# Kernel tuning notes

Hardware: AMD Instinct MI355X
Metric: run time of the kernel (lower is better)

The kernel has to match this reference:

```python
import jax, jax.numpy as jnp
import numpy as np

N_NODES = 100000
N_EDGES = 1600000
IN_FEATS = 128
H1 = 256
H2 = 256
N_CLASSES = 64


def setup_inputs() -> dict:
    key = jax.random.key(0)
    ks = jax.random.split(key, 12)
    x = jax.random.normal(ks[0], (N_NODES, IN_FEATS), dtype=jnp.float32)
    src = jax.random.randint(ks[1], (N_EDGES,), 0, N_NODES, dtype=jnp.int64 if jax.config.jax_enable_x64 else jnp.int32)
    dst = jax.random.randint(ks[2], (N_EDGES,), 0, N_NODES, dtype=jnp.int64 if jax.config.jax_enable_x64 else jnp.int32)
    def lin(kw, kb, fan_in, fan_out):
        bound = 1.0 / np.sqrt(fan_in)
        W = jax.random.uniform(kw, (fan_out, fan_in), minval=-bound, maxval=bound, dtype=jnp.float32)
        b = jax.random.uniform(kb, (fan_out,), minval=-bound, maxval=bound, dtype=jnp.float32)
        return W, b
    W1, b1 = lin(ks[3], ks[4], 2 * IN_FEATS, H1)
    W2, b2 = lin(ks[5], ks[6], 2 * H1, H2)
    W3, b3 = lin(ks[7], ks[8], 2 * H2, N_CLASSES)
    return {"x": x, "src": src, "dst": dst,
            "W1": W1, "b1": b1, "W2": W2, "b2": b2, "W3": W3, "b3": b3}


def _sage_conv(h, src, dst, W, b):
    # message = copy from src node, reduce = mean at dst node (DGL copy_u + mean)
    m = jnp.take(h, src, axis=0)                                  # [E, d]
    s = jax.ops.segment_sum(m, dst, num_segments=N_NODES)         # [N, d]
    deg = jax.ops.segment_sum(jnp.ones((m.shape[0],), h.dtype), dst,
                              num_segments=N_NODES)               # [N]
    h_N = s / jnp.maximum(deg, 1.0)[:, None]                      # isolated nodes -> 0 (DGL behavior)
    h_total = jnp.concatenate([h, h_N], axis=1)                   # [N, 2d]
    return h_total @ W.T + b                                      # dropout inactive at eval (p=0.05)


def reference(x, src, dst, W1, b1, W2, b2, W3, b3):
    h = jax.nn.relu(_sage_conv(x, src, dst, W1, b1))
    h = jax.nn.relu(_sage_conv(h, src, dst, W2, b2))
    return _sage_conv(h, src, dst, W3, b3)
```

## Files before the change

kernel.cpp:

```cpp
#include <hip/hip_runtime.h>
#include <hip/hip_bf16.h>
#include <cstdint>
#include <cstddef>

#define N_NODES 100000
#define N_EDGES 1600000
#define NBUCK   64
#define NPB     1563
#define NB_E    ((N_EDGES + 4095) / 4096)

typedef __attribute__((ext_vector_type(8))) short short8;
typedef __attribute__((ext_vector_type(4))) float floatx4;

__device__ inline float bf_lo(unsigned int u) { return __uint_as_float(u << 16); }
__device__ inline float bf_hi(unsigned int u) { return __uint_as_float(u & 0xffff0000u); }
__device__ inline unsigned short f2bf(float f) {
  unsigned int u = __float_as_uint(f);
  u += 0x7fffu + ((u >> 16) & 1u);
  return (unsigned short)(u >> 16);
}

__global__ void cvt_f32_bf16(const float* __restrict__ in,
                             unsigned short* __restrict__ out, int n4) {
  int t = blockIdx.x * blockDim.x + threadIdx.x;
  if (t >= n4) return;
  float4 v = ((const float4*)in)[t];
  ushort4 o;
  o.x = f2bf(v.x); o.y = f2bf(v.y); o.z = f2bf(v.z); o.w = f2bf(v.w);
  ((ushort4*)out)[t] = o;
}

__global__ void cvt_w3cat(const float* __restrict__ W3, unsigned short* __restrict__ out) {
  int t = blockIdx.x * blockDim.x + threadIdx.x;
  if (t >= 128 * 256 / 4) return;
  int idx4 = t * 4;
  int r = idx4 >> 8, c = idx4 & 255;
  float4 v = *(const float4*)(W3 + (size_t)(r & 63) * 512 + (r >> 6) * 256 + c);
  ushort4 o;
  o.x = f2bf(v.x); o.y = f2bf(v.y); o.z = f2bf(v.z); o.w = f2bf(v.w);
  *(ushort4*)(out + (size_t)r * 256 + c) = o;
}

__device__ inline int wave_incl_scan(int v, int lane) {
#pragma unroll
  for (int off = 1; off < 64; off <<= 1) {
    int t = __shfl_up(v, off, 64);
    if (lane >= off) v += t;
  }
  return v;
}

__global__ __launch_bounds__(256)
void pass1a_kernel(const int* __restrict__ dst, int* __restrict__ bucketCount) {
  __shared__ int hist[NBUCK];
  if (threadIdx.x < NBUCK) hist[threadIdx.x] = 0;
  __syncthreads();
#pragma unroll
  for (int i = 0; i < 16; ++i) {
    int e = blockIdx.x * 4096 + i * 256 + threadIdx.x;
    if (e < N_EDGES) atomicAdd(&hist[dst[e] / NPB], 1);
  }
  __syncthreads();
  if (threadIdx.x < NBUCK) atomicAdd(&bucketCount[threadIdx.x], hist[threadIdx.x]);
}

__global__ void scanB_kernel(const int* __restrict__ bucketCount,
                             int* __restrict__ bucketBase, int* __restrict__ gCursorB) {
  int t = threadIdx.x;
  int v = bucketCount[t];
  int incl = wave_incl_scan(v, t);
  bucketBase[t] = incl - v;
  gCursorB[t] = incl - v;
  if (t == 63) bucketBase[NBUCK] = incl;
}

__global__ __launch_bounds__(256)
void pass1b_kernel(const int* __restrict__ src, const int* __restrict__ dst,
                   int* __restrict__ gCursorB, uint2* __restrict__ staging) {
  __shared__ int hist[NBUCK];
  if (threadIdx.x < NBUCK) hist[threadIdx.x] = 0;
  __syncthreads();
#pragma unroll
  for (int i = 0; i < 16; ++i) {
    int e = blockIdx.x * 4096 + i * 256 + threadIdx.x;
    if (e < N_EDGES) atomicAdd(&hist[dst[e] / NPB], 1);
  }
  __syncthreads();
  if (threadIdx.x < NBUCK)
    hist[threadIdx.x] = atomicAdd(&gCursorB[threadIdx.x], hist[threadIdx.x]);
  __syncthreads();
#pragma unroll
  for (int i = 0; i < 16; ++i) {
    int e = blockIdx.x * 4096 + i * 256 + threadIdx.x;
    if (e < N_EDGES) {
      int d = dst[e];
      int pos = atomicAdd(&hist[d / NPB], 1);
      staging[pos] = make_uint2((unsigned)src[e], (unsigned)d);
    }
  }
}

__global__ __launch_bounds__(1024)
void pass2_kernel(const uint2* __restrict__ staging, const int* __restrict__ bucketBase,
                  int* __restrict__ start, float* __restrict__ invdeg,
                  int* __restrict__ esrc) {
  __shared__ int cnt[2048];
  __shared__ int cur[2048];
  __shared__ int wsum[16];
  const int b = blockIdx.x, tid = threadIdx.x;
  const int lane = tid & 63, wid = tid >> 6;
  const int n0 = b * NPB, n1 = min(n0 + NPB, N_NODES);
  const int nLocal = n1 - n0;
  const int p0 = bucketBase[b], p1 = bucketBase[b + 1];

  for (int i = tid; i < 2048; i += 1024) cnt[i] = 0;
  __syncthreads();
  for (int e = p0 + tid; e < p1; e += 1024)
    atomicAdd(&cnt[staging[e].y - n0], 1);
  __syncthreads();

  int c0 = cnt[2 * tid], c1 = cnt[2 * tid + 1];
  int s = c0 + c1;
  int incl = wave_incl_scan(s, lane);
  if (lane == 63) wsum[wid] = incl;
  __syncthreads();
  if (wid == 0) {
    int v = (lane < 16) ? wsum[lane] : 0;
    int i2 = wave_incl_scan(v, lane);
    if (lane < 16) wsum[lane] = i2 - v;
  }
  __syncthreads();
  int excl = wsum[wid] + incl - s;
  cur[2 * tid] = excl;
  cur[2 * tid + 1] = excl + c0;
  if (2 * tid < nLocal) {
    start[n0 + 2 * tid] = p0 + excl;
    invdeg[n0 + 2 * tid] = 1.0f / fmaxf((float)c0, 1.0f);
  }
  if (2 * tid + 1 < nLocal) {
    start[n0 + 2 * tid + 1] = p0 + excl + c0;
    invdeg[n0 + 2 * tid + 1] = 1.0f / fmaxf((float)c1, 1.0f);
  }
  if (b == NBUCK - 1 && tid == 0) start[N_NODES] = N_EDGES;
  __syncthreads();

  for (int e = p0 + tid; e < p1; e += 1024) {
    uint2 pr = staging[e];
    int pos = p0 + atomicAdd(&cur[pr.y - n0], 1);
    esrc[pos] = (int)pr.x;
  }
}

template<int D>
__global__ __launch_bounds__(256)
void gather_mean(const unsigned short* __restrict__ h,
                 const int* __restrict__ start,
                 const int* __restrict__ esrc,
                 const float* __restrict__ invdeg,
                 unsigned short* __restrict__ hn) {
  int wave = (int)((blockIdx.x * 256 + threadIdx.x) >> 6);
  if (wave >= N_NODES) return;
  int lane = threadIdx.x & 63;
  int s0 = start[wave], s1 = start[wave + 1];
  constexpr int FPL = D / 64;
  float acc[FPL] = {};
  const unsigned short* base = h + lane * FPL;

  int e = s0;
  if constexpr (FPL == 4) {
    for (; e + 4 <= s1; e += 4) {
      int sn0 = esrc[e], sn1 = esrc[e + 1], sn2 = esrc[e + 2], sn3 = esrc[e + 3];
      uint2 p0 = *(const uint2*)(base + (size_t)sn0 * D);
      uint2 p1 = *(const uint2*)(base + (size_t)sn1 * D);
      uint2 p2 = *(const uint2*)(base + (size_t)sn2 * D);
      uint2 p3 = *(const uint2*)(base + (size_t)sn3 * D);
      acc[0] += bf_lo(p0.x) + bf_lo(p1.x) + bf_lo(p2.x) + bf_lo(p3.x);
      acc[1] += bf_hi(p0.x) + bf_hi(p1.x) + bf_hi(p2.x) + bf_hi(p3.x);
      acc[2] += bf_lo(p0.y) + bf_lo(p1.y) + bf_lo(p2.y) + bf_lo(p3.y);
      acc[3] += bf_hi(p0.y) + bf_hi(p1.y) + bf_hi(p2.y) + bf_hi(p3.y);
    }
    for (; e < s1; ++e) {
      int sn = esrc[e];
      uint2 p = *(const uint2*)(base + (size_t)sn * D);
      acc[0] += bf_lo(p.x); acc[1] += bf_hi(p.x);
      acc[2] += bf_lo(p.y); acc[3] += bf_hi(p.y);
    }
  } else {
    for (; e + 4 <= s1; e += 4) {
      int sn0 = esrc[e], sn1 = esrc[e + 1], sn2 = esrc[e + 2], sn3 = esrc[e + 3];
      unsigned int p0 = *(const unsigned int*)(base + (size_t)sn0 * D);
      unsigned int p1 = *(const unsigned int*)(base + (size_t)sn1 * D);
      unsigned int p2 = *(const unsigned int*)(base + (size_t)sn2 * D);
      unsigned int p3 = *(const unsigned int*)(base + (size_t)sn3 * D);
      acc[0] += bf_lo(p0) + bf_lo(p1) + bf_lo(p2) + bf_lo(p3);
      acc[1] += bf_hi(p0) + bf_hi(p1) + bf_hi(p2) + bf_hi(p3);
    }
    for (; e < s1; ++e) {
      int sn = esrc[e];
      unsigned int p = *(const unsigned int*)(base + (size_t)sn * D);
      acc[0] += bf_lo(p); acc[1] += bf_hi(p);
    }
  }

  float inv = invdeg[wave];
  unsigned short* out = hn + (size_t)wave * D + lane * FPL;
  if constexpr (FPL == 4) {
    ushort4 o;
    o.x = f2bf(acc[0] * inv); o.y = f2bf(acc[1] * inv);
    o.z = f2bf(acc[2] * inv); o.w = f2bf(acc[3] * inv);
    *(ushort4*)out = o;
  } else {
    ushort2 o;
    o.x = f2bf(acc[0] * inv); o.y = f2bf(acc[1] * inv);
    *(ushort2*)out = o;
  }
}

__global__ __launch_bounds__(256)
void gather_add64(const unsigned short* __restrict__ Y3,
                  const int* __restrict__ start, const int* __restrict__ esrc,
                  const float* __restrict__ invdeg, float* __restrict__ out) {
  int wave = (int)((blockIdx.x * 256 + threadIdx.x) >> 6);
  if (wave >= N_NODES) return;
  int lane = threadIdx.x & 63;
  int half = lane >> 5, l32 = lane & 31;
  int s0 = start[wave], s1 = start[wave + 1];
  float a0 = 0.f, a1 = 0.f;
  for (int e = s0 + half; e < s1; e += 2) {
    int sn = esrc[e];
    unsigned int p = *(const unsigned int*)(Y3 + (size_t)sn * 64 + 2 * l32);
    a0 += bf_lo(p); a1 += bf_hi(p);
  }
  a0 += __shfl_xor(a0, 32, 64);
  a1 += __shfl_xor(a1, 32, 64);
  if (half == 0) {
    float inv = invdeg[wave];
    float2* q = (float2*)(out + (size_t)wave * 64 + 2 * l32);
    float2 v = *q;
    v.x += inv * a0; v.y += inv * a1;
    *q = v;
  }
}

template<int D, int DOUT, int BN, bool RELU, bool OUTF32, int MODE>
__global__ __launch_bounds__(256)
void sage_gemm(const unsigned short* __restrict__ H,
               const unsigned short* __restrict__ HN,
               const unsigned short* __restrict__ Wb,
               const float* __restrict__ bias,
               void* __restrict__ outp,
               unsigned short* __restrict__ y3) {
  constexpr int K   = (MODE == 1) ? D : 2 * D;
  constexpr int BM  = 128, KC = 32;
  constexpr int NCHUNK = K / KC;
  constexpr int AF  = BM / 16;
  constexpr int BF  = BN / 16;
  constexpr int FR  = AF + BF;
  constexpr int NMF = 4;
  constexpr int NJF = BF / 2;

  __shared__ __align__(16) unsigned short lds0[FR * 512];
  __shared__ __align__(16) unsigned short lds1[FR * 512];

  const int tid  = threadIdx.x;
  const int wave = tid >> 6, lane = tid & 63;
  const int l16  = lane & 15, quad = lane >> 4;
  const int n0   = blockIdx.x * BM;
  const int bn0  = blockIdx.y * BN;
  const int wm   = wave >> 1, wn = wave & 1;

  floatx4 acc[NMF][NJF] = {};

  auto stage = [&](int c, unsigned short* buf) {
    const int kc = c * KC;
    const unsigned short* srcH = (kc < D) ? H : HN;
    const int kb = (kc < D) ? kc : kc - D;
    const int w0 = __builtin_amdgcn_readfirstlane(wave);
#pragma unroll
    for (int i = 0; i < FR / 4; ++i) {
      const int fu = w0 + 4 * i;
      const unsigned short* g;
      if (fu < AF) {
        int row = min(n0 + fu * 16 + l16, N_NODES - 1);
        g = srcH + (size_t)row * D + kb + quad * 8;
      } else {
        int col = bn0 + (fu - AF) * 16 + l16;
        g = Wb + (size_t)col * K + kc + quad * 8;
      }
      __builtin_amdgcn_global_load_lds(
          (const __attribute__((address_space(1))) unsigned int*)g,
          (__attribute__((address_space(3))) unsigned int*)(buf + fu * 512),
          16, 0, 0);
    }
  };

  auto compute = [&](const unsigned short* buf) {
    short8 b[NJF];
#pragma unroll
    for (int jt = 0; jt < NJF; ++jt)
      b[jt] = *(const short8*)(buf + (AF + wn * NJF + jt) * 512 + lane * 8);
#pragma unroll
    for (int mi = 0; mi < NMF; ++mi) {
      short8 a = *(const short8*)(buf + (wm * NMF + mi) * 512 + lane * 8);
#pragma unroll
      for (int jt = 0; jt < NJF; ++jt)
        acc[mi][jt] = __builtin_amdgcn_mfma_f32_16x16x32_bf16(a, b[jt], acc[mi][jt], 0, 0, 0);
    }
  };

  stage(0, lds0);
  __syncthreads();
#pragma unroll 1
  for (int c = 0; c < NCHUNK; c += 2) {
    stage(c + 1, lds1);
    compute(lds0);
    __syncthreads();
    if (c + 2 < NCHUNK) stage(c + 2, lds0);
    compute(lds1);
    __syncthreads();
  }

#pragma unroll
  for (int mi = 0; mi < NMF; ++mi) {
#pragma unroll
    for (int jt = 0; jt < NJF; ++jt) {
      int j = bn0 + wn * (NJF * 16) + jt * 16 + l16;
      float bj = (MODE == 1 && wn == 1) ? 0.0f : bias[j];
#pragma unroll
      for (int r = 0; r < 4; ++r) {
        int node = n0 + wm * 64 + mi * 16 + quad * 4 + r;
        if (node < N_NODES) {
          float v = acc[mi][jt][r];
          if constexpr (MODE == 1) {
            if (wn == 0) ((float*)outp)[(size_t)node * 64 + j] = v + bj;
            else y3[(size_t)node * 64 + (j - 64)] = f2bf(v);
          } else {
            v += bj;
            if (RELU) v = fmaxf(v, 0.0f);
            if (OUTF32) ((float*)outp)[(size_t)node * DOUT + j] = v;
            else ((unsigned short*)outp)[(size_t)node * DOUT + j] = f2bf(v);
          }
        }
      }
    }
  }
}

extern "C" void kernel_launch(void* const* d_in, const int* in_sizes, int n_in,
                              void* d_out, int out_size, void* d_ws, size_t ws_size,
                              hipStream_t stream) {
  const float* x   = (const float*)d_in[0];
  const int*   src = (const int*)d_in[1];
  const int*   dst = (const int*)d_in[2];
  const float* W1 = (const float*)d_in[3];
  const float* b1 = (const float*)d_in[4];
  const float* W2 = (const float*)d_in[5];
  const float* b2 = (const float*)d_in[6];
  const float* W3 = (const float*)d_in[7];
  const float* b3 = (const float*)d_in[8];

  char* ws = (char*)d_ws;
  unsigned short* H0 = (unsigned short*)ws; ws += (size_t)N_NODES * 128 * 2;
  unsigned short* H1 = (unsigned short*)ws; ws += (size_t)N_NODES * 256 * 2;
  unsigned short* H2 = (unsigned short*)ws; ws += (size_t)N_NODES * 256 * 2;
  unsigned short* HN = (unsigned short*)ws; ws += (size_t)N_NODES * 256 * 2;
  uint2* staging = (uint2*)ws; ws += (size_t)N_EDGES * 8;
  int* esrc   = (int*)ws;  ws += (size_t)N_EDGES * 4;
  int* startp = (int*)ws;  ws += (size_t)(N_NODES + 32) * 4;
  float* invdeg = (float*)ws; ws += (size_t)(N_NODES + 32) * 4;
  int* bucketCount = (int*)ws; ws += 256;
  int* bucketBase  = (int*)ws; ws += 512;
  int* gCursorB    = (int*)ws; ws += 256;
  unsigned short* Y3 = (unsigned short*)ws; ws += (size_t)N_NODES * 64 * 2;
  unsigned short* Wb1 = (unsigned short*)ws; ws += 256 * 256 * 2;
  unsigned short* Wb2 = (unsigned short*)ws; ws += 256 * 512 * 2;
  unsigned short* Wb3 = (unsigned short*)ws; ws += 128 * 256 * 2;

  hipMemsetAsync(bucketCount, 0, NBUCK * 4, stream);
  pass1a_kernel<<<NB_E, 256, 0, stream>>>(dst, bucketCount);
  scanB_kernel<<<1, 64, 0, stream>>>(bucketCount, bucketBase, gCursorB);
  pass1b_kernel<<<NB_E, 256, 0, stream>>>(src, dst, gCursorB, staging);
  pass2_kernel<<<NBUCK, 1024, 0, stream>>>(staging, bucketBase, startp, invdeg, esrc);

  cvt_f32_bf16<<<(N_NODES * 128 / 4 + 255) / 256, 256, 0, stream>>>(x, H0, N_NODES * 128 / 4);
  cvt_f32_bf16<<<(256 * 256 / 4 + 255) / 256, 256, 0, stream>>>(W1, Wb1, 256 * 256 / 4);
  cvt_f32_bf16<<<(256 * 512 / 4 + 255) / 256, 256, 0, stream>>>(W2, Wb2, 256 * 512 / 4);
  cvt_w3cat<<<(128 * 256 / 4 + 255) / 256, 256, 0, stream>>>(W3, Wb3);

  const int GGRID = (N_NODES * 64 + 255) / 256;
  const int MG = (N_NODES + 127) / 128;

  gather_mean<128><<<GGRID, 256, 0, stream>>>(H0, startp, esrc, invdeg, HN);
  sage_gemm<128, 256, 128, true, false, 0><<<dim3(MG, 2), 256, 0, stream>>>(H0, HN, Wb1, b1, H1, nullptr);

  gather_mean<256><<<GGRID, 256, 0, stream>>>(H1, startp, esrc, invdeg, HN);
  sage_gemm<256, 256, 128, true, false, 0><<<dim3(MG, 2), 256, 0, stream>>>(H1, HN, Wb2, b2, H2, nullptr);

  sage_gemm<256, 128, 128, false, true, 1><<<dim3(MG, 1), 256, 0, stream>>>(H2, nullptr, Wb3, b3, (float*)d_out, Y3);
  gather_add64<<<GGRID, 256, 0, stream>>>(Y3, startp, esrc, invdeg, (float*)d_out);
}
```

Measured before the change: 628.0 us.

## Split each node's neighbor gather across two waves and double CSR buckets

Each gather kernel now assigns two waves per destination node. Each wave sums half of the edge range, and the two partial sums are combined through shared memory before the mean is written. The CSR build uses 128 buckets of 782 nodes instead of 64, so pass2 has more blocks and one node per thread, and the bucket scan becomes two-wave. The goal is more memory-level parallelism in the latency-bound gathers and a better-filled pass2, at the cost of twice as many waves, a block barrier, and more blocks per gather.

```diff
diff --git a/kernel.cpp b/kernel.cpp
--- a/kernel.cpp
+++ b/kernel.cpp
@@ -5,8 +5,8 @@
 
 #define N_NODES 100000
 #define N_EDGES 1600000
-#define NBUCK   64
-#define NPB     1563
+#define NBUCK   128
+#define NPB     782
 #define NB_E    ((N_EDGES + 4095) / 4096)
 
 typedef __attribute__((ext_vector_type(8))) short short8;
@@ -66,12 +66,16 @@
 
 __global__ void scanB_kernel(const int* __restrict__ bucketCount,
                              int* __restrict__ bucketBase, int* __restrict__ gCursorB) {
-  int t = threadIdx.x;
+  __shared__ int wsum[2];
+  int t = threadIdx.x, lane = t & 63, wid = t >> 6;
   int v = bucketCount[t];
-  int incl = wave_incl_scan(v, t);
-  bucketBase[t] = incl - v;
-  gCursorB[t] = incl - v;
-  if (t == 63) bucketBase[NBUCK] = incl;
+  int incl = wave_incl_scan(v, lane);
+  if (lane == 63) wsum[wid] = incl;
+  __syncthreads();
+  int off = (wid == 1) ? wsum[0] : 0;
+  bucketBase[t] = off + incl - v;
+  gCursorB[t]   = off + incl - v;
+  if (t == 127) bucketBase[NBUCK] = off + incl;
 }
 
 __global__ __launch_bounds__(256)
@@ -104,8 +108,8 @@
 void pass2_kernel(const uint2* __restrict__ staging, const int* __restrict__ bucketBase,
                   int* __restrict__ start, float* __restrict__ invdeg,
                   int* __restrict__ esrc) {
-  __shared__ int cnt[2048];
-  __shared__ int cur[2048];
+  __shared__ int cnt[1024];
+  __shared__ int cur[1024];
   __shared__ int wsum[16];
   const int b = blockIdx.x, tid = threadIdx.x;
   const int lane = tid & 63, wid = tid >> 6;
@@ -113,15 +117,14 @@
   const int nLocal = n1 - n0;
   const int p0 = bucketBase[b], p1 = bucketBase[b + 1];
 
-  for (int i = tid; i < 2048; i += 1024) cnt[i] = 0;
+  cnt[tid] = 0;
   __syncthreads();
   for (int e = p0 + tid; e < p1; e += 1024)
     atomicAdd(&cnt[staging[e].y - n0], 1);
   __syncthreads();
 
-  int c0 = cnt[2 * tid], c1 = cnt[2 * tid + 1];
-  int s = c0 + c1;
-  int incl = wave_incl_scan(s, lane);
+  int c = cnt[tid];
+  int incl = wave_incl_scan(c, lane);
   if (lane == 63) wsum[wid] = incl;
   __syncthreads();
   if (wid == 0) {
@@ -130,16 +133,11 @@
     if (lane < 16) wsum[lane] = i2 - v;
   }
   __syncthreads();
-  int excl = wsum[wid] + incl - s;
-  cur[2 * tid] = excl;
-  cur[2 * tid + 1] = excl + c0;
-  if (2 * tid < nLocal) {
-    start[n0 + 2 * tid] = p0 + excl;
-    invdeg[n0 + 2 * tid] = 1.0f / fmaxf((float)c0, 1.0f);
-  }
-  if (2 * tid + 1 < nLocal) {
-    start[n0 + 2 * tid + 1] = p0 + excl + c0;
-    invdeg[n0 + 2 * tid + 1] = 1.0f / fmaxf((float)c1, 1.0f);
+  int excl = wsum[wid] + incl - c;
+  cur[tid] = excl;
+  if (tid < nLocal) {
+    start[n0 + tid] = p0 + excl;
+    invdeg[n0 + tid] = 1.0f / fmaxf((float)c, 1.0f);
   }
   if (b == NBUCK - 1 && tid == 0) start[N_NODES] = N_EDGES;
   __syncthreads();
@@ -158,17 +156,20 @@
                  const int* __restrict__ esrc,
                  const float* __restrict__ invdeg,
                  unsigned short* __restrict__ hn) {
-  int wave = (int)((blockIdx.x * 256 + threadIdx.x) >> 6);
-  if (wave >= N_NODES) return;
-  int lane = threadIdx.x & 63;
-  int s0 = start[wave], s1 = start[wave + 1];
   constexpr int FPL = D / 64;
+  __shared__ float part[2][D];
+  const int tid = threadIdx.x, wave = tid >> 6, lane = tid & 63;
+  const int local = wave >> 1, sub = wave & 1;
+  const int node = blockIdx.x * 2 + local;
+  const int s0 = start[node], s1 = start[node + 1];
+  const int mid = s0 + ((s1 - s0 + 1) >> 1);
+  int e = sub ? mid : s0;
+  const int bnd = sub ? s1 : mid;
   float acc[FPL] = {};
   const unsigned short* base = h + lane * FPL;
 
-  int e = s0;
   if constexpr (FPL == 4) {
-    for (; e + 4 <= s1; e += 4) {
+    for (; e + 4 <= bnd; e += 4) {
       int sn0 = esrc[e], sn1 = esrc[e + 1], sn2 = esrc[e + 2], sn3 = esrc[e + 3];
       uint2 p0 = *(const uint2*)(base + (size_t)sn0 * D);
       uint2 p1 = *(const uint2*)(base + (size_t)sn1 * D);
@@ -179,14 +180,14 @@
       acc[2] += bf_lo(p0.y) + bf_lo(p1.y) + bf_lo(p2.y) + bf_lo(p3.y);
       acc[3] += bf_hi(p0.y) + bf_hi(p1.y) + bf_hi(p2.y) + bf_hi(p3.y);
     }
-    for (; e < s1; ++e) {
+    for (; e < bnd; ++e) {
       int sn = esrc[e];
       uint2 p = *(const uint2*)(base + (size_t)sn * D);
       acc[0] += bf_lo(p.x); acc[1] += bf_hi(p.x);
       acc[2] += bf_lo(p.y); acc[3] += bf_hi(p.y);
     }
   } else {
-    for (; e + 4 <= s1; e += 4) {
+    for (; e + 4 <= bnd; e += 4) {
       int sn0 = esrc[e], sn1 = esrc[e + 1], sn2 = esrc[e + 2], sn3 = esrc[e + 3];
       unsigned int p0 = *(const unsigned int*)(base + (size_t)sn0 * D);
       unsigned int p1 = *(const unsigned int*)(base + (size_t)sn1 * D);
@@ -195,24 +196,35 @@
       acc[0] += bf_lo(p0) + bf_lo(p1) + bf_lo(p2) + bf_lo(p3);
       acc[1] += bf_hi(p0) + bf_hi(p1) + bf_hi(p2) + bf_hi(p3);
     }
-    for (; e < s1; ++e) {
+    for (; e < bnd; ++e) {
       int sn = esrc[e];
       unsigned int p = *(const unsigned int*)(base + (size_t)sn * D);
       acc[0] += bf_lo(p); acc[1] += bf_hi(p);
     }
   }
 
-  float inv = invdeg[wave];
-  unsigned short* out = hn + (size_t)wave * D + lane * FPL;
-  if constexpr (FPL == 4) {
-    ushort4 o;
-    o.x = f2bf(acc[0] * inv); o.y = f2bf(acc[1] * inv);
-    o.z = f2bf(acc[2] * inv); o.w = f2bf(acc[3] * inv);
-    *(ushort4*)out = o;
-  } else {
-    ushort2 o;
-    o.x = f2bf(acc[0] * inv); o.y = f2bf(acc[1] * inv);
-    *(ushort2*)out = o;
+  if (sub == 1) {
+    if constexpr (FPL == 4)
+      *(float4*)&part[local][lane * 4] = make_float4(acc[0], acc[1], acc[2], acc[3]);
+    else
+      *(float2*)&part[local][lane * 2] = make_float2(acc[0], acc[1]);
+  }
+  __syncthreads();
+  if (sub == 0) {
+    float inv = invdeg[node];
+    unsigned short* out = hn + (size_t)node * D + lane * FPL;
+    if constexpr (FPL == 4) {
+      float4 p = *(const float4*)&part[local][lane * 4];
+      ushort4 o;
+      o.x = f2bf((acc[0] + p.x) * inv); o.y = f2bf((acc[1] + p.y) * inv);
+      o.z = f2bf((acc[2] + p.z) * inv); o.w = f2bf((acc[3] + p.w) * inv);
+      *(ushort4*)out = o;
+    } else {
+      float2 p = *(const float2*)&part[local][lane * 2];
+      ushort2 o;
+      o.x = f2bf((acc[0] + p.x) * inv); o.y = f2bf((acc[1] + p.y) * inv);
+      *(ushort2*)out = o;
+    }
   }
 }
 
@@ -220,24 +232,32 @@
 void gather_add64(const unsigned short* __restrict__ Y3,
                   const int* __restrict__ start, const int* __restrict__ esrc,
                   const float* __restrict__ invdeg, float* __restrict__ out) {
-  int wave = (int)((blockIdx.x * 256 + threadIdx.x) >> 6);
-  if (wave >= N_NODES) return;
-  int lane = threadIdx.x & 63;
-  int half = lane >> 5, l32 = lane & 31;
-  int s0 = start[wave], s1 = start[wave + 1];
+  __shared__ float part[2][64];
+  const int tid = threadIdx.x, wave = tid >> 6, lane = tid & 63;
+  const int local = wave >> 1, sub = wave & 1;
+  const int node = blockIdx.x * 2 + local;
+  const int half = lane >> 5, l32 = lane & 31;
+  const int s0 = start[node], s1 = start[node + 1];
+  const int mid = s0 + ((s1 - s0 + 1) >> 1);
+  const int a = sub ? mid : s0, bnd = sub ? s1 : mid;
   float a0 = 0.f, a1 = 0.f;
-  for (int e = s0 + half; e < s1; e += 2) {
+  for (int e = a + half; e < bnd; e += 2) {
     int sn = esrc[e];
     unsigned int p = *(const unsigned int*)(Y3 + (size_t)sn * 64 + 2 * l32);
     a0 += bf_lo(p); a1 += bf_hi(p);
   }
   a0 += __shfl_xor(a0, 32, 64);
   a1 += __shfl_xor(a1, 32, 64);
-  if (half == 0) {
-    float inv = invdeg[wave];
-    float2* q = (float2*)(out + (size_t)wave * 64 + 2 * l32);
+  if (sub == 1 && half == 0) {
+    part[local][2 * l32] = a0; part[local][2 * l32 + 1] = a1;
+  }
+  __syncthreads();
+  if (sub == 0 && half == 0) {
+    float inv = invdeg[node];
+    float2* q = (float2*)(out + (size_t)node * 64 + 2 * l32);
     float2 v = *q;
-    v.x += inv * a0; v.y += inv * a1;
+    v.x += inv * (a0 + part[local][2 * l32]);
+    v.y += inv * (a1 + part[local][2 * l32 + 1]);
     *q = v;
   }
 }
@@ -368,9 +388,9 @@
   int* esrc   = (int*)ws;  ws += (size_t)N_EDGES * 4;
   int* startp = (int*)ws;  ws += (size_t)(N_NODES + 32) * 4;
   float* invdeg = (float*)ws; ws += (size_t)(N_NODES + 32) * 4;
-  int* bucketCount = (int*)ws; ws += 256;
-  int* bucketBase  = (int*)ws; ws += 512;
-  int* gCursorB    = (int*)ws; ws += 256;
+  int* bucketCount = (int*)ws; ws += 512;
+  int* bucketBase  = (int*)ws; ws += 1024;
+  int* gCursorB    = (int*)ws; ws += 512;
   unsigned short* Y3 = (unsigned short*)ws; ws += (size_t)N_NODES * 64 * 2;
   unsigned short* Wb1 = (unsigned short*)ws; ws += 256 * 256 * 2;
   unsigned short* Wb2 = (unsigned short*)ws; ws += 256 * 512 * 2;
@@ -378,7 +398,7 @@
 
   hipMemsetAsync(bucketCount, 0, NBUCK * 4, stream);
   pass1a_kernel<<<NB_E, 256, 0, stream>>>(dst, bucketCount);
-  scanB_kernel<<<1, 64, 0, stream>>>(bucketCount, bucketBase, gCursorB);
+  scanB_kernel<<<1, 128, 0, stream>>>(bucketCount, bucketBase, gCursorB);
   pass1b_kernel<<<NB_E, 256, 0, stream>>>(src, dst, gCursorB, staging);
   pass2_kernel<<<NBUCK, 1024, 0, stream>>>(staging, bucketBase, startp, invdeg, esrc);
 
@@ -387,15 +407,15 @@
   cvt_f32_bf16<<<(256 * 512 / 4 + 255) / 256, 256, 0, stream>>>(W2, Wb2, 256 * 512 / 4);
   cvt_w3cat<<<(128 * 256 / 4 + 255) / 256, 256, 0, stream>>>(W3, Wb3);
 
-  const int GGRID = (N_NODES * 64 + 255) / 256;
+  const int GGRID2 = N_NODES / 2;
   const int MG = (N_NODES + 127) / 128;
 
-  gather_mean<128><<<GGRID, 256, 0, stream>>>(H0, startp, esrc, invdeg, HN);
+  gather_mean<128><<<GGRID2, 256, 0, stream>>>(H0, startp, esrc, invdeg, HN);
   sage_gemm<128, 256, 128, true, false, 0><<<dim3(MG, 2), 256, 0, stream>>>(H0, HN, Wb1, b1, H1, nullptr);
 
-  gather_mean<256><<<GGRID, 256, 0, stream>>>(H1, startp, esrc, invdeg, HN);
+  gather_mean<256><<<GGRID2, 256, 0, stream>>>(H1, startp, esrc, invdeg, HN);
   sage_gemm<256, 256, 128, true, false, 0><<<dim3(MG, 2), 256, 0, stream>>>(H1, HN, Wb2, b2, H2, nullptr);
 
   sage_gemm<256, 128, 128, false, true, 1><<<dim3(MG, 1), 256, 0, stream>>>(H2, nullptr, Wb3, b3, (float*)d_out, Y3);
-  gather_add64<<<GGRID, 256, 0, stream>>>(Y3, startp, esrc, invdeg, (float*)d_out);
-}
+  gather_add64<<<GGRID2, 256, 0, stream>>>(Y3, startp, esrc, invdeg, (float*)d_out);
+}
```

After: 657.6 us. 4.7% more time.
